# Performance work log

Hardware: AMD Instinct MI355X
Metric: run time of the kernel (lower is better)

The kernel has to match this reference:

```python
import jax, jax.numpy as jnp
import numpy as np

N = 65536
E = 1048576
IN_DIM, HID, OUT = 500, 256, 64
ALPHA = 0.1
K = 10


def setup_inputs() -> dict:
    key = jax.random.key(0)
    ks = jax.random.split(key, 12)
    x = jax.random.normal(ks[0], (N, IN_DIM), dtype=jnp.float32)
    edge_row = jax.random.randint(ks[1], (E,), 0, N, dtype=jnp.int32)
    edge_col = jax.random.randint(ks[2], (E,), 0, N, dtype=jnp.int32)
    edge_weight = jax.random.uniform(ks[3], (E,), dtype=jnp.float32)
    # Linear params (Kaiming-uniform-like scale)
    def lin(k, fan_in, fan_out):
        kw, kb = jax.random.split(k)
        bound = 1.0 / np.sqrt(fan_in)
        W = jax.random.uniform(kw, (fan_in, fan_out), minval=-bound, maxval=bound, dtype=jnp.float32)
        b = jax.random.uniform(kb, (fan_out,), minval=-bound, maxval=bound, dtype=jnp.float32)
        return W, b
    W1, b1 = lin(ks[4], IN_DIM, HID)
    W2, b2 = lin(ks[5], HID, HID)
    W3, b3 = lin(ks[6], HID, OUT)
    return {"x": x, "W1": W1, "b1": b1, "W2": W2, "b2": b2,
            "W3": W3, "b3": b3, "edge_weight": edge_weight,
            "edge_row": edge_row, "edge_col": edge_col}


def reference(x, W1, b1, W2, b2, W3, b3, edge_weight, edge_row, edge_col):
    # MLP stack (dropout=0.0, norm_type='none')
    h = jax.nn.relu(x @ W1 + b1)          # [N, HID]
    h = jax.nn.relu(h @ W2 + b2)          # [N, HID]
    h = h @ W3 + b3                        # [N, OUT]
    h0 = h
    w = edge_weight[:, None]               # [E, 1]
    # APPNP: k steps of h = (1-alpha) * (A @ h) + alpha * h0 (SpMM via segment_sum)
    def step(h, _):
        msg = h[edge_col] * w               # [E, OUT] gather + scale
        agg = jax.ops.segment_sum(msg, edge_row, num_segments=N)  # [N, OUT]
        return (1.0 - ALPHA) * agg + ALPHA * h0, None
    h, _ = jax.lax.scan(step, h, None, length=K)
    return h
```

## Files before the change

### kernel.cpp

```cpp
#include <hip/hip_runtime.h>
#include <cstdint>
#include <cstddef>


#define N_NODES   65536
#define N_EDGES   1048576
#define IN_DIM    500
#define IN_PAD    512
#define HID_DIM   256
#define OUT_DIM   64
#define K_STEPS   10

#define NPW   8
#define CAPW  608
#define NCHUNK 16

typedef _Float16 half8 __attribute__((ext_vector_type(8)));
typedef float    f32x4 __attribute__((ext_vector_type(4)));

#define XB_OFF    0ULL
#define HA_OFF    0ULL
#define HB_OFF    33554432ULL
#define H1_OFF    67108864ULL
#define H0_OFF    67108864ULL
#define H2_OFF    100663296ULL
#define CNT2_OFF  100663296ULL
#define RANK_OFF  104857600ULL
#define TOT_OFF   109051904ULL
#define W1T_OFF   134217728ULL
#define W2T_OFF   134479872ULL
#define W3T_OFF   134610944ULL
#define ROWP_OFF  134643712ULL
#define EDG_OFF   135430400ULL

__device__ __forceinline__ void gload_lds16(const void* g, void* l) {
  __builtin_amdgcn_global_load_lds(
      (const __attribute__((address_space(1))) void*)g,
      (__attribute__((address_space(3))) void*)l, 16, 0, 0);
}

__device__ __forceinline__ float bf2f(unsigned short u) {
  return __uint_as_float(((unsigned)u) << 16);
}
__device__ __forceinline__ unsigned short f2bf_rne(float f) {
  unsigned u = __float_as_uint(f);
  u += 0x7fffu + ((u >> 16) & 1u);
  return (unsigned short)(u >> 16);
}
__device__ __forceinline__ float uaf(int u) {
  return __uint_as_float((unsigned)u);
}

template <int TM, int TN, int WM, int WN, bool RELU, int OMODE>
__global__ __launch_bounds__(256)
void gemm_kernel(const _Float16* __restrict__ A, const _Float16* __restrict__ B,
                 const float* __restrict__ bias, void* __restrict__ Cout,
                 int M, int Nn, int K) {
  static_assert((TM * 8) % 256 == 0 && (TN * 8) % 256 == 0, "tile");
  __shared__ uint4 As[TM * 8];
  __shared__ uint4 Bs[TN * 8];
  const int t    = threadIdx.x;
  const int lane = t & 63;
  const int wave = t >> 6;
  const int wm   = wave / WN;
  const int wn   = wave % WN;
  const int row0 = blockIdx.x * TM;
  const int col0 = blockIdx.y * TN;
  const int l15  = lane & 15;
  const int lq   = lane >> 4;

  f32x4 acc[4][4];
#pragma unroll
  for (int i = 0; i < 4; ++i)
#pragma unroll
    for (int j = 0; j < 4; ++j) acc[i][j] = (f32x4){0.f, 0.f, 0.f, 0.f};

  for (int k0 = 0; k0 < K; k0 += 64) {
#pragma unroll
    for (int i = 0; i < (TM * 8) / 256; ++i) {
      const int c = i * 256 + wave * 64 + lane;
      const int q = c / TM;
      const int r = c % TM;
      gload_lds16(A + (size_t)(row0 + r) * K + (k0 + q * 8),
                  As + i * 256 + wave * 64);
    }
#pragma unroll
    for (int i = 0; i < (TN * 8) / 256; ++i) {
      const int c = i * 256 + wave * 64 + lane;
      const int q = c / TN;
      const int r = c % TN;
      gload_lds16(B + (size_t)(col0 + r) * K + (k0 + q * 8),
                  Bs + i * 256 + wave * 64);
    }
    __syncthreads();
#pragma unroll
    for (int kk = 0; kk < 2; ++kk) {
      const int qa = kk * 4 + lq;
      half8 af[4], bfr[4];
#pragma unroll
      for (int mt = 0; mt < 4; ++mt)
        af[mt] = *((const half8*)(As + (qa * TM + wm * 64 + mt * 16 + l15)));
#pragma unroll
      for (int nt = 0; nt < 4; ++nt)
        bfr[nt] = *((const half8*)(Bs + (qa * TN + wn * 64 + nt * 16 + l15)));
#pragma unroll
      for (int mt = 0; mt < 4; ++mt)
#pragma unroll
        for (int nt = 0; nt < 4; ++nt)
          acc[mt][nt] = __builtin_amdgcn_mfma_f32_16x16x32_f16(
              af[mt], bfr[nt], acc[mt][nt], 0, 0, 0);
    }
    __syncthreads();
  }

#pragma unroll
  for (int mt = 0; mt < 4; ++mt) {
#pragma unroll
    for (int nt = 0; nt < 4; ++nt) {
      const int col = col0 + wn * 64 + nt * 16 + l15;
      const float bv = bias[col];
#pragma unroll
      for (int r = 0; r < 4; ++r) {
        const int row = row0 + wm * 64 + mt * 16 + lq * 4 + r;
        float v = acc[mt][nt][r] + bv;
        if (RELU) v = fmaxf(v, 0.f);
        if (OMODE == 0)
          ((_Float16*)Cout)[(size_t)row * Nn + col] = (_Float16)v;
        else if (OMODE == 1)
          ((unsigned short*)Cout)[(size_t)row * Nn + col] = f2bf_rne(v);
        else
          ((float*)Cout)[(size_t)row * Nn + col] = v;
      }
    }
  }
}

__global__ void cast_x_kernel(const float* __restrict__ x,
                              _Float16* __restrict__ xb) {
  const int c = blockIdx.x * blockDim.x + threadIdx.x;
  if (c >= N_NODES * (IN_PAD / 8)) return;
  const int row = c >> 6;
  const int c8  = (c & 63) << 3;
  half8 o;
  if (c8 + 8 <= IN_DIM) {
    const float4* p = (const float4*)(x + (size_t)row * IN_DIM + c8);
    const float4 a = p[0], b = p[1];
    o[0] = (_Float16)a.x; o[1] = (_Float16)a.y;
    o[2] = (_Float16)a.z; o[3] = (_Float16)a.w;
    o[4] = (_Float16)b.x; o[5] = (_Float16)b.y;
    o[6] = (_Float16)b.z; o[7] = (_Float16)b.w;
  } else {
#pragma unroll
    for (int j = 0; j < 8; ++j) {
      const float v = (c8 + j < IN_DIM) ? x[(size_t)row * IN_DIM + c8 + j] : 0.f;
      o[j] = (_Float16)v;
    }
  }
  *(half8*)(xb + (size_t)c * 8) = o;
}

__global__ void cast_w_kernel(const float* __restrict__ W,
                              _Float16* __restrict__ Wt, int K, int Kpad,
                              int Nn) {
  const int idx = blockIdx.x * blockDim.x + threadIdx.x;
  if (idx >= Nn * Kpad) return;
  const int n = idx / Kpad;
  const int k = idx % Kpad;
  const float v = (k < K) ? W[(size_t)k * Nn + n] : 0.f;
  Wt[idx] = (_Float16)v;
}

__global__ void hist2_kernel(const int* __restrict__ row,
                             int* __restrict__ cnt2, int* __restrict__ rank,
                             int E) {
  const int e = blockIdx.x * blockDim.x + threadIdx.x;
  if (e < E)
    rank[e] = atomicAdd(&cnt2[(e >> 16) * N_NODES + row[e]], 1);
}

__global__ void scan_tot_kernel(const int* __restrict__ cnt2,
                                int* __restrict__ tot) {
  const int r = blockIdx.x * blockDim.x + threadIdx.x;
  int s = 0;
#pragma unroll
  for (int c = 0; c < NCHUNK; ++c) s += cnt2[c * N_NODES + r];
  tot[r] = s;
}

__global__ void scan_kernel(const int4* __restrict__ counts4,
                            int* __restrict__ rowptr) {
  __shared__ int part[1024];
  const int t = threadIdx.x;
  const int base = t * 16;
  int4 c[16];
  int s = 0;
#pragma unroll
  for (int i = 0; i < 16; ++i) {
    c[i] = counts4[base + i];
    s += c[i].x + c[i].y + c[i].z + c[i].w;
  }
  part[t] = s;
  __syncthreads();
  for (int off = 1; off < 1024; off <<= 1) {
    const int v = (t >= off) ? part[t - off] : 0;
    __syncthreads();
    part[t] += v;
    __syncthreads();
  }
  int run = (t == 0) ? 0 : part[t - 1];
#pragma unroll
  for (int i = 0; i < 16; ++i) {
    int4 r;
    r.x = run; run += c[i].x;
    r.y = run; run += c[i].y;
    r.z = run; run += c[i].z;
    r.w = run; run += c[i].w;
    ((int4*)rowptr)[base + i] = r;
  }
  if (t == 1023) rowptr[N_NODES] = run;
}

__global__ void chunkbase_kernel(int* __restrict__ cnt2,
                                 const int* __restrict__ rowptr) {
  const int r = blockIdx.x * blockDim.x + threadIdx.x;
  int run = rowptr[r];
#pragma unroll
  for (int c = 0; c < NCHUNK; ++c) {
    const int t = cnt2[c * N_NODES + r];
    cnt2[c * N_NODES + r] = run;
    run += t;
  }
}

__global__ void scatter2_kernel(const int* __restrict__ row,
                                const int* __restrict__ col,
                                const float* __restrict__ w,
                                const int* __restrict__ rank,
                                const int* __restrict__ cbase,
                                int2* __restrict__ edges, int E) {
  const int e = blockIdx.x * blockDim.x + threadIdx.x;
  if (e < E) {
    const int pos = cbase[(e >> 16) * N_NODES + row[e]] + rank[e];
    edges[pos] = make_int2(col[e], __float_as_int(w[e]));
  }
}

template <bool OUT_F32>
__global__ __launch_bounds__(256)
void prop_step(const unsigned short* __restrict__ hin,
               const unsigned short* __restrict__ h0,
               void* __restrict__ hout, const int* __restrict__ rowptr,
               const int2* __restrict__ edges) {
  __shared__ int2 eb[4][CAPW];
  const int wave = threadIdx.x >> 6;
  const int lane = threadIdx.x & 63;
  const int node0 = (blockIdx.x * 4 + wave) * NPW;

  const int rp  = rowptr[node0 + min(lane, NPW)];
  const int beg = __shfl(rp, 0);
  const int nE  = __shfl(rp, NPW) - beg;
  const int rrel = rp - beg;
  int2* __restrict__ ebw = eb[wave];

  const bool fast = (nE <= CAPW);
  if (fast) {
    for (int i = lane; i < nE; i += 64) ebw[i] = edges[beg + i];
    __builtin_amdgcn_s_waitcnt(0);
  }

  for (int i = 0; i < NPW; ++i) {
    const int nb = __shfl(rrel, i);
    const int ne = __shfl(rrel, i + 1);
    float a0 = 0.f, a1 = 0.f, a2 = 0.f, a3 = 0.f;
    if (fast) {
      int j = nb;
      for (; j + 8 <= ne; j += 8) {
        const int2 e0 = ebw[j + 0];
        const int2 e1 = ebw[j + 1];
        const int2 e2 = ebw[j + 2];
        const int2 e3 = ebw[j + 3];
        const int2 e4 = ebw[j + 4];
        const int2 e5 = ebw[j + 5];
        const int2 e6 = ebw[j + 6];
        const int2 e7 = ebw[j + 7];
        const float v0 = bf2f(hin[((size_t)e0.x << 6) | lane]);
        const float v1 = bf2f(hin[((size_t)e1.x << 6) | lane]);
        const float v2 = bf2f(hin[((size_t)e2.x << 6) | lane]);
        const float v3 = bf2f(hin[((size_t)e3.x << 6) | lane]);
        const float v4 = bf2f(hin[((size_t)e4.x << 6) | lane]);
        const float v5 = bf2f(hin[((size_t)e5.x << 6) | lane]);
        const float v6 = bf2f(hin[((size_t)e6.x << 6) | lane]);
        const float v7 = bf2f(hin[((size_t)e7.x << 6) | lane]);
        a0 = fmaf(uaf(e0.y), v0, a0);
        a1 = fmaf(uaf(e1.y), v1, a1);
        a2 = fmaf(uaf(e2.y), v2, a2);
        a3 = fmaf(uaf(e3.y), v3, a3);
        a0 = fmaf(uaf(e4.y), v4, a0);
        a1 = fmaf(uaf(e5.y), v5, a1);
        a2 = fmaf(uaf(e6.y), v6, a2);
        a3 = fmaf(uaf(e7.y), v7, a3);
      }
      for (; j + 4 <= ne; j += 4) {
        const int2 e0 = ebw[j + 0];
        const int2 e1 = ebw[j + 1];
        const int2 e2 = ebw[j + 2];
        const int2 e3 = ebw[j + 3];
        const float v0 = bf2f(hin[((size_t)e0.x << 6) | lane]);
        const float v1 = bf2f(hin[((size_t)e1.x << 6) | lane]);
        const float v2 = bf2f(hin[((size_t)e2.x << 6) | lane]);
        const float v3 = bf2f(hin[((size_t)e3.x << 6) | lane]);
        a0 = fmaf(uaf(e0.y), v0, a0);
        a1 = fmaf(uaf(e1.y), v1, a1);
        a2 = fmaf(uaf(e2.y), v2, a2);
        a3 = fmaf(uaf(e3.y), v3, a3);
      }
      for (; j < ne; ++j) {
        const int2 e = ebw[j];
        a0 = fmaf(uaf(e.y), bf2f(hin[((size_t)e.x << 6) | lane]), a0);
      }
    } else {
      for (int j = nb; j < ne; ++j) {
        const int2 e = edges[beg + j];
        a0 = fmaf(uaf(e.y), bf2f(hin[((size_t)e.x << 6) | lane]), a0);
      }
    }
    const float acc = (a0 + a1) + (a2 + a3);
    const size_t o = ((size_t)(node0 + i) << 6) | lane;
    const float r = 0.9f * acc + 0.1f * bf2f(h0[o]);
    if (OUT_F32)
      ((float*)hout)[o] = r;
    else
      ((unsigned short*)hout)[o] = f2bf_rne(r);
  }
}

extern "C" void kernel_launch(void* const* d_in, const int* in_sizes, int n_in,
                              void* d_out, int out_size, void* d_ws,
                              size_t ws_size, hipStream_t stream) {
  const float* x  = (const float*)d_in[0];
  const float* W1 = (const float*)d_in[1];
  const float* b1 = (const float*)d_in[2];
  const float* W2 = (const float*)d_in[3];
  const float* b2 = (const float*)d_in[4];
  const float* W3 = (const float*)d_in[5];
  const float* b3 = (const float*)d_in[6];
  const float* ew = (const float*)d_in[7];
  const int* erow = (const int*)d_in[8];
  const int* ecol = (const int*)d_in[9];

  char* ws = (char*)d_ws;
  _Float16* xb  = (_Float16*)(ws + XB_OFF);
  _Float16* h1  = (_Float16*)(ws + H1_OFF);
  _Float16* h2  = (_Float16*)(ws + H2_OFF);
  _Float16* w1t = (_Float16*)(ws + W1T_OFF);
  _Float16* w2t = (_Float16*)(ws + W2T_OFF);
  _Float16* w3t = (_Float16*)(ws + W3T_OFF);
  unsigned short* h0b = (unsigned short*)(ws + H0_OFF);
  unsigned short* hAb = (unsigned short*)(ws + HA_OFF);
  unsigned short* hBb = (unsigned short*)(ws + HB_OFF);
  int* rowp     = (int*)(ws + ROWP_OFF);
  int* cnt2     = (int*)(ws + CNT2_OFF);
  int* rankb    = (int*)(ws + RANK_OFF);
  int* tot      = (int*)(ws + TOT_OFF);
  int2* edges   = (int2*)(ws + EDG_OFF);
  float* outp   = (float*)d_out;

  hipMemsetAsync(cnt2, 0, NCHUNK * N_NODES * sizeof(int), stream);
  hist2_kernel<<<N_EDGES / 256, 256, 0, stream>>>(erow, cnt2, rankb, N_EDGES);
  scan_tot_kernel<<<N_NODES / 256, 256, 0, stream>>>(cnt2, tot);
  scan_kernel<<<1, 1024, 0, stream>>>((const int4*)tot, rowp);
  chunkbase_kernel<<<N_NODES / 256, 256, 0, stream>>>(cnt2, rowp);
  scatter2_kernel<<<N_EDGES / 256, 256, 0, stream>>>(erow, ecol, ew, rankb,
                                                     cnt2, edges, N_EDGES);

  cast_x_kernel<<<(N_NODES * (IN_PAD / 8)) / 256, 256, 0, stream>>>(x, xb);
  cast_w_kernel<<<(HID_DIM * IN_PAD) / 256, 256, 0, stream>>>(W1, w1t, IN_DIM,
                                                              IN_PAD, HID_DIM);
  cast_w_kernel<<<(HID_DIM * HID_DIM) / 256, 256, 0, stream>>>(
      W2, w2t, HID_DIM, HID_DIM, HID_DIM);
  cast_w_kernel<<<(OUT_DIM * HID_DIM) / 256, 256, 0, stream>>>(
      W3, w3t, HID_DIM, HID_DIM, OUT_DIM);

  gemm_kernel<128, 128, 2, 2, true, 0>
      <<<dim3(N_NODES / 128, HID_DIM / 128), 256, 0, stream>>>(
          xb, w1t, b1, h1, N_NODES, HID_DIM, IN_PAD);
  gemm_kernel<128, 128, 2, 2, true, 0>
      <<<dim3(N_NODES / 128, HID_DIM / 128), 256, 0, stream>>>(
          h1, w2t, b2, h2, N_NODES, HID_DIM, HID_DIM);
  gemm_kernel<256, 64, 4, 1, false, 1>
      <<<dim3(N_NODES / 256, 1), 256, 0, stream>>>(h2, w3t, b3, h0b, N_NODES,
                                                   OUT_DIM, HID_DIM);

  for (int s = 0; s < K_STEPS - 1; ++s) {
    const unsigned short* hin = (s == 0) ? h0b : ((s - 1) & 1 ? hBb : hAb);
    unsigned short* hout = (s & 1) ? hBb : hAb;
    prop_step<false><<<N_NODES / (4 * NPW), 256, 0, stream>>>(hin, h0b, hout,
                                                              rowp, edges);
  }
  prop_step<true><<<N_NODES / (4 * NPW), 256, 0, stream>>>(
      (K_STEPS - 2) & 1 ? hBb : hAb, h0b, outp, rowp, edges);
}
```

Baseline: 658.2 us.

## Split propagation into two 32-feature slab passes with half-wave edge parallelism

The 64-wide bf16 feature matrix is re-laid out as two column-major slabs of 32 features, each node row being 64 bytes. Each propagation step now runs as two kernel passes, one per slab, so the gather working set per pass is half the size and is more likely to stay resident in cache. Inside a pass each half-wave handles alternate edges and the two halves are combined with a cross-lane shuffle. Non-temporal loads and stores are used for the edge list, h0 and the outputs. The cost is twice as many launches and twice the edge-list reads per step.

```diff
diff --git a/kernel.cpp b/kernel.cpp
--- a/kernel.cpp
+++ b/kernel.cpp
@@ -14,6 +14,7 @@
 #define NPW   8
 #define CAPW  608
 #define NCHUNK 16
+#define SLAB  (N_NODES * 32)
 
 typedef _Float16 half8 __attribute__((ext_vector_type(8)));
 typedef float    f32x4 __attribute__((ext_vector_type(4)));
@@ -126,10 +127,11 @@
         if (RELU) v = fmaxf(v, 0.f);
         if (OMODE == 0)
           ((_Float16*)Cout)[(size_t)row * Nn + col] = (_Float16)v;
-        else if (OMODE == 1)
-          ((unsigned short*)Cout)[(size_t)row * Nn + col] = f2bf_rne(v);
+        else if (OMODE == 2)
+          ((float*)Cout)[(size_t)row * Nn + col] = v;
         else
-          ((float*)Cout)[(size_t)row * Nn + col] = v;
+          ((unsigned short*)Cout)[((size_t)(col >> 5) * M + row) * 32 +
+                                  (col & 31)] = f2bf_rne(v);
       }
     }
   }
@@ -247,13 +249,15 @@
 
 template <bool OUT_F32>
 __global__ __launch_bounds__(256)
-void prop_step(const unsigned short* __restrict__ hin,
-               const unsigned short* __restrict__ h0,
-               void* __restrict__ hout, const int* __restrict__ rowptr,
-               const int2* __restrict__ edges) {
+void prop_split(const unsigned short* __restrict__ hin,
+                const unsigned short* __restrict__ h0,
+                void* __restrict__ hout, const int* __restrict__ rowptr,
+                const int2* __restrict__ edges, int pass) {
   __shared__ int2 eb[4][CAPW];
   const int wave = threadIdx.x >> 6;
   const int lane = threadIdx.x & 63;
+  const int g    = lane >> 5;
+  const int f    = lane & 31;
   const int node0 = (blockIdx.x * 4 + wave) * NPW;
 
   const int rp  = rowptr[node0 + min(lane, NPW)];
@@ -262,75 +266,65 @@
   const int rrel = rp - beg;
   int2* __restrict__ ebw = eb[wave];
 
-  const bool fast = (nE <= CAPW);
-  if (fast) {
-    for (int i = lane; i < nE; i += 64) ebw[i] = edges[beg + i];
+  const bool fastp = (nE <= CAPW);
+  if (fastp) {
+    const unsigned long long* src = (const unsigned long long*)(edges + beg);
+    for (int i = lane; i < nE; i += 64) {
+      const unsigned long long v = __builtin_nontemporal_load(src + i);
+      *(unsigned long long*)&ebw[i] = v;
+    }
     __builtin_amdgcn_s_waitcnt(0);
   }
 
   for (int i = 0; i < NPW; ++i) {
     const int nb = __shfl(rrel, i);
     const int ne = __shfl(rrel, i + 1);
+    const int cnt = ne - nb;
     float a0 = 0.f, a1 = 0.f, a2 = 0.f, a3 = 0.f;
-    if (fast) {
-      int j = nb;
-      for (; j + 8 <= ne; j += 8) {
-        const int2 e0 = ebw[j + 0];
-        const int2 e1 = ebw[j + 1];
-        const int2 e2 = ebw[j + 2];
-        const int2 e3 = ebw[j + 3];
-        const int2 e4 = ebw[j + 4];
-        const int2 e5 = ebw[j + 5];
-        const int2 e6 = ebw[j + 6];
-        const int2 e7 = ebw[j + 7];
-        const float v0 = bf2f(hin[((size_t)e0.x << 6) | lane]);
-        const float v1 = bf2f(hin[((size_t)e1.x << 6) | lane]);
-        const float v2 = bf2f(hin[((size_t)e2.x << 6) | lane]);
-        const float v3 = bf2f(hin[((size_t)e3.x << 6) | lane]);
-        const float v4 = bf2f(hin[((size_t)e4.x << 6) | lane]);
-        const float v5 = bf2f(hin[((size_t)e5.x << 6) | lane]);
-        const float v6 = bf2f(hin[((size_t)e6.x << 6) | lane]);
-        const float v7 = bf2f(hin[((size_t)e7.x << 6) | lane]);
-        a0 = fmaf(uaf(e0.y), v0, a0);
-        a1 = fmaf(uaf(e1.y), v1, a1);
-        a2 = fmaf(uaf(e2.y), v2, a2);
-        a3 = fmaf(uaf(e3.y), v3, a3);
-        a0 = fmaf(uaf(e4.y), v4, a0);
-        a1 = fmaf(uaf(e5.y), v5, a1);
-        a2 = fmaf(uaf(e6.y), v6, a2);
-        a3 = fmaf(uaf(e7.y), v7, a3);
+    if (fastp) {
+      int t = 0;
+      for (; t + 8 <= cnt; t += 8) {
+        const int2 E0 = ebw[nb + t + 0 + g];
+        const int2 E1 = ebw[nb + t + 2 + g];
+        const int2 E2 = ebw[nb + t + 4 + g];
+        const int2 E3 = ebw[nb + t + 6 + g];
+        const float v0 = bf2f(hin[((size_t)E0.x << 5) + f]);
+        const float v1 = bf2f(hin[((size_t)E1.x << 5) + f]);
+        const float v2 = bf2f(hin[((size_t)E2.x << 5) + f]);
+        const float v3 = bf2f(hin[((size_t)E3.x << 5) + f]);
+        a0 = fmaf(uaf(E0.y), v0, a0);
+        a1 = fmaf(uaf(E1.y), v1, a1);
+        a2 = fmaf(uaf(E2.y), v2, a2);
+        a3 = fmaf(uaf(E3.y), v3, a3);
       }
-      for (; j + 4 <= ne; j += 4) {
-        const int2 e0 = ebw[j + 0];
-        const int2 e1 = ebw[j + 1];
-        const int2 e2 = ebw[j + 2];
-        const int2 e3 = ebw[j + 3];
-        const float v0 = bf2f(hin[((size_t)e0.x << 6) | lane]);
-        const float v1 = bf2f(hin[((size_t)e1.x << 6) | lane]);
-        const float v2 = bf2f(hin[((size_t)e2.x << 6) | lane]);
-        const float v3 = bf2f(hin[((size_t)e3.x << 6) | lane]);
-        a0 = fmaf(uaf(e0.y), v0, a0);
-        a1 = fmaf(uaf(e1.y), v1, a1);
-        a2 = fmaf(uaf(e2.y), v2, a2);
-        a3 = fmaf(uaf(e3.y), v3, a3);
-      }
-      for (; j < ne; ++j) {
-        const int2 e = ebw[j];
-        a0 = fmaf(uaf(e.y), bf2f(hin[((size_t)e.x << 6) | lane]), a0);
+      for (; t < cnt; t += 2) {
+        const int idx = t + g;
+        const bool act = idx < cnt;
+        const int2 E = ebw[nb + (act ? idx : 0)];
+        const float w = act ? uaf(E.y) : 0.f;
+        a0 = fmaf(w, bf2f(hin[((size_t)E.x << 5) + f]), a0);
       }
     } else {
-      for (int j = nb; j < ne; ++j) {
-        const int2 e = edges[beg + j];
-        a0 = fmaf(uaf(e.y), bf2f(hin[((size_t)e.x << 6) | lane]), a0);
+      for (int t = 0; t < cnt; t += 2) {
+        const int idx = t + g;
+        const bool act = idx < cnt;
+        const int2 E = edges[beg + nb + (act ? idx : 0)];
+        const float w = act ? uaf(E.y) : 0.f;
+        a0 = fmaf(w, bf2f(hin[((size_t)E.x << 5) + f]), a0);
       }
     }
-    const float acc = (a0 + a1) + (a2 + a3);
-    const size_t o = ((size_t)(node0 + i) << 6) | lane;
-    const float r = 0.9f * acc + 0.1f * bf2f(h0[o]);
-    if (OUT_F32)
-      ((float*)hout)[o] = r;
-    else
-      ((unsigned short*)hout)[o] = f2bf_rne(r);
+    float acc = (a0 + a1) + (a2 + a3);
+    acc += __shfl_xor(acc, 32);
+    const size_t so = ((size_t)(node0 + i) << 5) + f;
+    const unsigned short h0v = __builtin_nontemporal_load(h0 + so);
+    const float r = 0.9f * acc + 0.1f * bf2f(h0v);
+    if (lane < 32) {
+      if (OUT_F32)
+        __builtin_nontemporal_store(
+            r, (float*)hout + ((size_t)(node0 + i) << 6) + (pass << 5) + f);
+      else
+        __builtin_nontemporal_store(f2bf_rne(r), (unsigned short*)hout + so);
+    }
   }
 }
 
@@ -387,16 +381,24 @@
   gemm_kernel<128, 128, 2, 2, true, 0>
       <<<dim3(N_NODES / 128, HID_DIM / 128), 256, 0, stream>>>(
           h1, w2t, b2, h2, N_NODES, HID_DIM, HID_DIM);
-  gemm_kernel<256, 64, 4, 1, false, 1>
+  gemm_kernel<256, 64, 4, 1, false, 3>
       <<<dim3(N_NODES / 256, 1), 256, 0, stream>>>(h2, w3t, b3, h0b, N_NODES,
                                                    OUT_DIM, HID_DIM);
 
-  for (int s = 0; s < K_STEPS - 1; ++s) {
+  const int PB = N_NODES / (4 * NPW);
+  for (int s = 0; s < K_STEPS; ++s) {
     const unsigned short* hin = (s == 0) ? h0b : ((s - 1) & 1 ? hBb : hAb);
     unsigned short* hout = (s & 1) ? hBb : hAb;
-    prop_step<false><<<N_NODES / (4 * NPW), 256, 0, stream>>>(hin, h0b, hout,
-                                                              rowp, edges);
-  }
-  prop_step<true><<<N_NODES / (4 * NPW), 256, 0, stream>>>(
-      (K_STEPS - 2) & 1 ? hBb : hAb, h0b, outp, rowp, edges);
-}
+    const bool last = (s == K_STEPS - 1);
+    for (int p = 0; p < 2; ++p) {
+      const unsigned short* hin_p = hin + (size_t)p * SLAB;
+      const unsigned short* h0_p  = h0b + (size_t)p * SLAB;
+      if (last)
+        prop_split<true><<<PB, 256, 0, stream>>>(hin_p, h0_p, outp, rowp,
+                                                 edges, p);
+      else
+        prop_split<false><<<PB, 256, 0, stream>>>(
+            hin_p, h0_p, hout + (size_t)p * SLAB, rowp, edges, p);
+    }
+  }
+}
```

After: 923.0 us. +40.2%, slower.
